# Optimization experiments

Measured on AMD Instinct MI355X. Metric: run time of the kernel, lower is better.

The kernel has to match this reference:

```python
import jax, jax.numpy as jnp
import numpy as np

B, C, H, W = 8, 256, 48, 48
EPS = 1e-5  # BatchNorm2d default eps


def setup_inputs() -> dict:
    key = jax.random.key(0)
    ks = jax.random.split(key, 8)
    return {
        "Q_feat_s": jax.random.normal(ks[0], (B, C, H, W), dtype=jnp.float32),
        "KV_feat_s": jax.random.normal(ks[1], (B, C, H, W), dtype=jnp.float32),
        "Wq": jax.random.normal(ks[2], (C, C), dtype=jnp.float32) * 0.02,
        "Wk": jax.random.normal(ks[3], (C, C), dtype=jnp.float32) * 0.02,
        "Wv": jax.random.normal(ks[4], (C, C), dtype=jnp.float32) * 0.02,
        "Wz": jax.random.normal(ks[5], (C, C), dtype=jnp.float32) * 0.02,
        "bn_gamma": jnp.ones((C,), dtype=jnp.float32),
        "bn_beta": jnp.zeros((C,), dtype=jnp.float32),
        "bn_mean": jax.random.normal(ks[6], (C,), dtype=jnp.float32) * 0.1,
        "bn_var": jax.random.uniform(ks[7], (C,), dtype=jnp.float32, minval=0.5, maxval=1.5),
    }


def reference(Q_feat_s, KV_feat_s, Wq, Wk, Wv, Wz, bn_gamma, bn_beta, bn_mean, bn_var):
    b, c, h, w = Q_feat_s.shape
    n = h * w
    # 1x1 convs == channel-mixing matmuls
    Q = jnp.einsum('oc,bchw->bohw', Wq, Q_feat_s).reshape(b, c, n)      # [B,C,N]
    K = jnp.einsum('oc,bchw->bohw', Wk, KV_feat_s).reshape(b, c, n)     # [B,C,N]
    V = jnp.einsum('oc,bchw->bohw', Wv, KV_feat_s).reshape(b, c, n)     # [B,C,N]
    # attn = (Q^T K)/N then @ V^T; linear (no softmax) so reassociate: Q^T (K V^T)/N
    KV = jnp.einsum('bcn,bdn->bcd', K, V) / n                           # [B,C,C]
    QKV = jnp.einsum('bcn,bcd->bdn', Q, KV)                             # [B,C,N]
    x = QKV.reshape(b, c, h, w)
    # W_z 1x1 conv + BatchNorm2d (inference / running stats)
    z = jnp.einsum('oc,bchw->bohw', Wz, x)
    inv = bn_gamma / jnp.sqrt(bn_var + EPS)
    z = z * inv[None, :, None, None] + (bn_beta - bn_mean * inv)[None, :, None, None]
    return z + Q_feat_s
```

## Files before the change

kernel.cpp:

```cpp
#include <hip/hip_runtime.h>

#define Bv 8
#define Cc 256
#define Nn 2304
#define EPS 1e-5f

typedef float f32x4 __attribute__((ext_vector_type(4)));
typedef __bf16 bf16x8 __attribute__((ext_vector_type(8)));

static __device__ __forceinline__ f32x4 mfma16(bf16x8 a, bf16x8 b, f32x4 c) {
    return __builtin_amdgcn_mfma_f32_16x16x32_bf16(a, b, c, 0, 0, 0);
}

static __device__ __forceinline__ bf16x8 cvt8(float4 a, float4 b) {
    bf16x8 r;
    r[0] = (__bf16)a.x; r[1] = (__bf16)a.y; r[2] = (__bf16)a.z; r[3] = (__bf16)a.w;
    r[4] = (__bf16)b.x; r[5] = (__bf16)b.y; r[6] = (__bf16)b.z; r[7] = (__bf16)b.w;
    return r;
}

static __device__ __forceinline__ bf16x8 load_cvt8(const float* __restrict__ p) {
    return cvt8(*(const float4*)p, *(const float4*)(p + 4));
}

static __device__ __forceinline__ bf16x8 load4_add_cvt8(
    const float* __restrict__ p0, const float* __restrict__ p1,
    const float* __restrict__ p2, const float* __restrict__ p3) {
    float4 x0 = *(const float4*)p0, x1 = *(const float4*)(p0 + 4);
    float4 y0 = *(const float4*)p1, y1 = *(const float4*)(p1 + 4);
    float4 z0 = *(const float4*)p2, z1 = *(const float4*)(p2 + 4);
    float4 w0 = *(const float4*)p3, w1 = *(const float4*)(p3 + 4);
    bf16x8 r;
    r[0] = (__bf16)(x0.x + y0.x + z0.x + w0.x);
    r[1] = (__bf16)(x0.y + y0.y + z0.y + w0.y);
    r[2] = (__bf16)(x0.z + y0.z + z0.z + w0.z);
    r[3] = (__bf16)(x0.w + y0.w + z0.w + w0.w);
    r[4] = (__bf16)(x1.x + y1.x + z1.x + w1.x);
    r[5] = (__bf16)(x1.y + y1.y + z1.y + w1.y);
    r[6] = (__bf16)(x1.z + y1.z + z1.z + w1.z);
    r[7] = (__bf16)(x1.w + y1.w + z1.w + w1.w);
    return r;
}

static __device__ __forceinline__ bf16x8 load_add_cvt8(const float* __restrict__ p0,
                                                       const float* __restrict__ p1) {
    float4 a0 = *(const float4*)p0;
    float4 a1 = *(const float4*)(p0 + 4);
    float4 b0 = *(const float4*)p1;
    float4 b1 = *(const float4*)(p1 + 4);
    bf16x8 r;
    r[0] = (__bf16)(a0.x + b0.x); r[1] = (__bf16)(a0.y + b0.y);
    r[2] = (__bf16)(a0.z + b0.z); r[3] = (__bf16)(a0.w + b0.w);
    r[4] = (__bf16)(a1.x + b1.x); r[5] = (__bf16)(a1.y + b1.y);
    r[6] = (__bf16)(a1.z + b1.z); r[7] = (__bf16)(a1.w + b1.w);
    return r;
}

__global__ __launch_bounds__(256) void k_front(
    const float* __restrict__ KVf,
    const float* __restrict__ Wq, const float* __restrict__ Wk,
    const float* __restrict__ Wv, const float* __restrict__ Wz,
    const float* __restrict__ gamma, const float* __restrict__ var_,
    unsigned short* __restrict__ Lb_us, unsigned short* __restrict__ Rtb_us,
    float* __restrict__ Spart) {
    __shared__ __align__(16) char smem[32768];
    int blk = blockIdx.x, tid = threadIdx.x;

    if (blk < 512) {
        __bf16 (*As)[72] = (__bf16 (*)[72])smem;
        __bf16 (*Bs)[72] = (__bf16 (*)[72])(smem + 9216);
        int b = blk & 7;
        int tt = (blk >> 3) & 15;
        int kc = blk >> 7;
        int tr = (tt >> 2) * 64, tc = (tt & 3) * 64;
        int k0 = kc * 576;
        int l = tid & 63, w = tid >> 6;
        int lr = l & 15, kofs = (l >> 4) * 8;
        int row = tid >> 2, c0 = (tid & 3) * 16;
        const float* Ap = KVf + ((size_t)b * Cc + tr + row) * Nn + k0 + c0;
        const float* Bp = KVf + ((size_t)b * Cc + tc + row) * Nn + k0 + c0;
        float4 fa0, fa1, fa2, fa3, fb0, fb1, fb2, fb3;
#define LD_TILE(ks) do { \
        const float* ap_ = Ap + (ks) * 64; \
        const float* bp_ = Bp + (ks) * 64; \
        fa0 = *(const float4*)ap_;         fa1 = *(const float4*)(ap_ + 4); \
        fa2 = *(const float4*)(ap_ + 8);   fa3 = *(const float4*)(ap_ + 12); \
        fb0 = *(const float4*)bp_;         fb1 = *(const float4*)(bp_ + 4); \
        fb2 = *(const float4*)(bp_ + 8);   fb3 = *(const float4*)(bp_ + 12); \
    } while (0)
        f32x4 zero = {0.f, 0.f, 0.f, 0.f};
        f32x4 acc[4] = {zero, zero, zero, zero};
        LD_TILE(0);
        for (int ks = 0; ks < 9; ++ks) {
            *(bf16x8*)&As[row][c0]     = cvt8(fa0, fa1);
            *(bf16x8*)&As[row][c0 + 8] = cvt8(fa2, fa3);
            *(bf16x8*)&Bs[row][c0]     = cvt8(fb0, fb1);
            *(bf16x8*)&Bs[row][c0 + 8] = cvt8(fb2, fb3);
            __syncthreads();
            if (ks < 8) LD_TILE(ks + 1);
#pragma unroll
            for (int kk = 0; kk < 64; kk += 32) {
                bf16x8 af = *(const bf16x8*)&As[w * 16 + lr][kk + kofs];
#pragma unroll
                for (int j = 0; j < 4; ++j) {
                    bf16x8 bb = *(const bf16x8*)&Bs[j * 16 + lr][kk + kofs];
                    acc[j] = mfma16(af, bb, acc[j]);
                }
            }
            __syncthreads();
        }
#undef LD_TILE
        float* Sp = Spart + ((size_t)kc * Bv + b) * 65536;
        int row0 = tr + w * 16 + ((l >> 4) << 2);
#pragma unroll
        for (int j = 0; j < 4; ++j) {
            int col = tc + j * 16 + lr;
#pragma unroll
            for (int r = 0; r < 4; ++r)
                Sp[(size_t)(row0 + r) * 256 + col] = acc[j][r];
        }
    } else {
        float* bufA = (float*)smem;
        float* bufB = bufA + 4096;
        __bf16* Lb  = (__bf16*)Lb_us;
        __bf16* Rtb = (__bf16*)Rtb_us;
        int wblk = blk - 512;
        bool isL = (wblk < 256);
        int t = isL ? wblk : wblk - 256;
        int tr = (t >> 4) * 16, tc = (t & 15) * 16;
        if (isL) {
            for (int idx = tid; idx < 4096; idx += 256) {
                int r = idx >> 8, m = idx & 255;
                bufA[idx] = Wz[(tr + r) * 256 + m];
            }
            for (int idx = tid; idx < 4096; idx += 256) {
                int m = idx >> 4, j = idx & 15;
                bufB[idx] = Wv[m * 256 + tc + j];
            }
        } else {
            for (int idx = tid; idx < 4096; idx += 256) {
                int o = idx >> 4, j = idx & 15;
                bufA[idx] = Wq[o * 256 + tr + j];
                bufB[idx] = Wk[o * 256 + tc + j];
            }
        }
        __syncthreads();
        int oo = tid >> 4, cc = tid & 15;
        float sum = 0.f;
        if (isL) {
#pragma unroll 8
            for (int m = 0; m < 256; ++m) sum += bufA[oo * 256 + m] * bufB[m * 16 + cc];
            int o = tr + oo;
            float inv = gamma[o] / sqrtf(var_[o] + EPS);
            Lb[o * 256 + tc + cc] = (__bf16)(inv * sum * (1.0f / (float)Nn));
        } else {
#pragma unroll 8
            for (int o = 0; o < 256; ++o) sum += bufA[o * 16 + oo] * bufB[o * 16 + cc];
            Rtb[(tr + oo) * 256 + tc + cc] = (__bf16)sum;
        }
    }
}

__global__ __launch_bounds__(256) void k_mid1(
    const unsigned short* __restrict__ Lb_us, const float* __restrict__ Spart,
    float* __restrict__ Tpart) {
    const __bf16* Lb = (const __bf16*)Lb_us;
    int blk = blockIdx.x;
    int b = blk & 7;
    int t = (blk >> 3) & 15;
    int kc = blk >> 7;
    int tr = (t >> 2) * 64, tc = (t & 3) * 64;
    int k0 = kc * 128;
    int tid = threadIdx.x, l = tid & 63, w = tid >> 6;
    int lr = l & 15, kofs = (l >> 4) * 8;
    const float* S0 = Spart + (size_t)(0 * Bv + b) * 65536;
    const float* S1 = Spart + (size_t)(1 * Bv + b) * 65536;
    const float* S2 = Spart + (size_t)(2 * Bv + b) * 65536;
    const float* S3 = Spart + (size_t)(3 * Bv + b) * 65536;
    f32x4 zero = {0.f, 0.f, 0.f, 0.f};
    f32x4 acc[4] = {zero, zero, zero, zero};
    int arow = tr + w * 16 + lr;
    for (int kk = 0; kk < 128; kk += 32) {
        bf16x8 af = *(const bf16x8*)&Lb[arow * 256 + k0 + kk + kofs];
#pragma unroll
        for (int j = 0; j < 4; ++j) {
            size_t boff = (size_t)(tc + j * 16 + lr) * 256 + k0 + kk + kofs;
            bf16x8 bb = load4_add_cvt8(S0 + boff, S1 + boff, S2 + boff, S3 + boff);
            acc[j] = mfma16(af, bb, acc[j]);
        }
    }
    float* Tp = Tpart + ((size_t)kc * Bv + b) * 65536;
    int row0 = tr + w * 16 + ((l >> 4) << 2);
#pragma unroll
    for (int j = 0; j < 4; ++j) {
        int col = tc + j * 16 + lr;
#pragma unroll
        for (int r = 0; r < 4; ++r)
            Tp[(size_t)(row0 + r) * 256 + col] = acc[j][r];
    }
}

__global__ __launch_bounds__(256) void k_mid2(
    const float* __restrict__ Tpart, const unsigned short* __restrict__ Rtb_us,
    unsigned short* __restrict__ Pb_us) {
    const __bf16* Rtb = (const __bf16*)Rtb_us;
    __bf16* Pb = (__bf16*)Pb_us;
    int blk = blockIdx.x;
    int b = blk & 7;
    int t = blk >> 3;
    int tr = (t >> 2) * 64, tc = (t & 3) * 64;
    int tid = threadIdx.x, l = tid & 63, w = tid >> 6;
    int lr = l & 15, kofs = (l >> 4) * 8;
    const float* T0 = Tpart + (size_t)b * 65536;
    const float* T1 = Tpart + (size_t)(Bv + b) * 65536;
    f32x4 zero = {0.f, 0.f, 0.f, 0.f};
    f32x4 acc[4] = {zero, zero, zero, zero};
    int arow = tr + w * 16 + lr;
    for (int kk = 0; kk < 256; kk += 32) {
        bf16x8 af = load_add_cvt8(&T0[(size_t)arow * 256 + kk + kofs],
                                  &T1[(size_t)arow * 256 + kk + kofs]);
#pragma unroll
        for (int j = 0; j < 4; ++j) {
            int brow = tc + j * 16 + lr;
            bf16x8 bb = *(const bf16x8*)&Rtb[brow * 256 + kk + kofs];
            acc[j] = mfma16(af, bb, acc[j]);
        }
    }
    __bf16* Pbb = Pb + ((size_t)b << 16);
    int row0 = tr + w * 16 + ((l >> 4) << 2);
#pragma unroll
    for (int j = 0; j < 4; ++j) {
        int col = tc + j * 16 + lr;
#pragma unroll
        for (int r = 0; r < 4; ++r)
            Pbb[(size_t)(row0 + r) * 256 + col] = (__bf16)acc[j][r];
    }
}

__global__ __launch_bounds__(512) void k_out(
    const unsigned short* __restrict__ Pb_us, const float* __restrict__ Qf,
    const float* __restrict__ gamma, const float* __restrict__ beta,
    const float* __restrict__ mean, const float* __restrict__ var_,
    float* __restrict__ out) {
    __shared__ __bf16 Qs[64][264];
    const __bf16* Pb = (const __bf16*)Pb_us;
    int bid = blockIdx.x;
    int b = bid & 7, nt = bid >> 3;
    int n0 = nt * 64;
    int tid = threadIdx.x, l = tid & 63, w = tid >> 6;
    int lr = l & 15, kofs = (l >> 4) * 8;

    const float* src = Qf + (size_t)b * Cc * Nn + n0;
    for (int idx = tid; idx < 4096; idx += 512) {
        int c = idx >> 4, ng = (idx & 15) << 2;
        float4 v = *(const float4*)(src + (size_t)c * Nn + ng);
        Qs[ng + 0][c] = (__bf16)v.x;
        Qs[ng + 1][c] = (__bf16)v.y;
        Qs[ng + 2][c] = (__bf16)v.z;
        Qs[ng + 3][c] = (__bf16)v.w;
    }
    __syncthreads();

    int obase = w * 32;
    const __bf16* A = Pb + ((size_t)b << 16);
    f32x4 zero = {0.f, 0.f, 0.f, 0.f};
    f32x4 acc[2][4];
#pragma unroll
    for (int i = 0; i < 2; ++i)
#pragma unroll
        for (int j = 0; j < 4; ++j) acc[i][j] = zero;

    for (int kk = 0; kk < 256; kk += 32) {
        bf16x8 af[2], bb[4];
#pragma unroll
        for (int i = 0; i < 2; ++i)
            af[i] = *(const bf16x8*)&A[(size_t)(obase + i * 16 + lr) * 256 + kk + kofs];
#pragma unroll
        for (int j = 0; j < 4; ++j)
            bb[j] = *(const bf16x8*)&Qs[j * 16 + lr][kk + kofs];
#pragma unroll
        for (int i = 0; i < 2; ++i)
#pragma unroll
            for (int j = 0; j < 4; ++j)
                acc[i][j] = mfma16(af[i], bb[j], acc[i][j]);
    }

    const float* Qfb = Qf + (size_t)b * Cc * Nn;
    float* outb = out + (size_t)b * Cc * Nn;
#pragma unroll
    for (int i = 0; i < 2; ++i) {
        int o0 = obase + i * 16 + ((l >> 4) << 2);
#pragma unroll
        for (int r = 0; r < 4; ++r) {
            int o = o0 + r;
            float inv = gamma[o] / sqrtf(var_[o] + EPS);
            float shift = beta[o] - mean[o] * inv;
#pragma unroll
            for (int j = 0; j < 4; ++j) {
                int n = n0 + j * 16 + lr;
                outb[(size_t)o * Nn + n] = acc[i][j][r] + shift + Qfb[(size_t)o * Nn + n];
            }
        }
    }
}

extern "C" void kernel_launch(void* const* d_in, const int* in_sizes, int n_in,
                              void* d_out, int out_size, void* d_ws, size_t ws_size,
                              hipStream_t stream) {
    (void)in_sizes; (void)n_in; (void)out_size; (void)ws_size;
    const float* Qf    = (const float*)d_in[0];
    const float* KVf   = (const float*)d_in[1];
    const float* Wq    = (const float*)d_in[2];
    const float* Wk    = (const float*)d_in[3];
    const float* Wv    = (const float*)d_in[4];
    const float* Wz    = (const float*)d_in[5];
    const float* gamma = (const float*)d_in[6];
    const float* beta  = (const float*)d_in[7];
    const float* mean  = (const float*)d_in[8];
    const float* var_  = (const float*)d_in[9];
    float* out = (float*)d_out;

    char* ws = (char*)d_ws;
    float* Spart        = (float*)ws;
    float* Tpart        = (float*)(ws + (8u << 20));
    unsigned short* Lb  = (unsigned short*)(ws + (12u << 20));
    unsigned short* Rtb = (unsigned short*)(ws + (12u << 20) + (128u << 10));
    unsigned short* Pb  = (unsigned short*)(ws + (12u << 20) + (256u << 10));

    k_front<<<1024, 256, 0, stream>>>(KVf, Wq, Wk, Wv, Wz, gamma, var_,
                                      Lb, Rtb, Spart);
    k_mid1<<<256, 256, 0, stream>>>(Lb, Spart, Tpart);
    k_mid2<<<128, 256, 0, stream>>>(Tpart, Rtb, Pb);
    k_out<<<288, 512, 0, stream>>>(Pb, Qf, gamma, beta, mean, var_, out);
}
```

Before: 156.5 us.

## Fuse two middle GEMM kernels via LDS row strips and halve k_out tile width

Merges k_mid1 and k_mid2 into one kernel. Each block computes a 16-row strip of the L·S product over the full K, stages it in shared memory as bf16, then multiplies by Rt to produce Pb. This removes the fp32 Tpart split-K partials round-trip through global memory and one launch, at the cost of fewer blocks (128) and each block re-reading the full S (summing four partials). The output kernel's N tile also shrinks from 64 to 32 columns, doubling its grid to 576 blocks for more parallelism while reloading Pb more often.

```diff
diff --git a/kernel.cpp b/kernel.cpp
--- a/kernel.cpp
+++ b/kernel.cpp
@@ -17,10 +17,6 @@
     r[0] = (__bf16)a.x; r[1] = (__bf16)a.y; r[2] = (__bf16)a.z; r[3] = (__bf16)a.w;
     r[4] = (__bf16)b.x; r[5] = (__bf16)b.y; r[6] = (__bf16)b.z; r[7] = (__bf16)b.w;
     return r;
-}
-
-static __device__ __forceinline__ bf16x8 load_cvt8(const float* __restrict__ p) {
-    return cvt8(*(const float4*)p, *(const float4*)(p + 4));
 }
 
 static __device__ __forceinline__ bf16x8 load4_add_cvt8(
@@ -39,20 +35,6 @@
     r[5] = (__bf16)(x1.y + y1.y + z1.y + w1.y);
     r[6] = (__bf16)(x1.z + y1.z + z1.z + w1.z);
     r[7] = (__bf16)(x1.w + y1.w + z1.w + w1.w);
-    return r;
-}
-
-static __device__ __forceinline__ bf16x8 load_add_cvt8(const float* __restrict__ p0,
-                                                       const float* __restrict__ p1) {
-    float4 a0 = *(const float4*)p0;
-    float4 a1 = *(const float4*)(p0 + 4);
-    float4 b0 = *(const float4*)p1;
-    float4 b1 = *(const float4*)(p1 + 4);
-    bf16x8 r;
-    r[0] = (__bf16)(a0.x + b0.x); r[1] = (__bf16)(a0.y + b0.y);
-    r[2] = (__bf16)(a0.z + b0.z); r[3] = (__bf16)(a0.w + b0.w);
-    r[4] = (__bf16)(a1.x + b1.x); r[5] = (__bf16)(a1.y + b1.y);
-    r[6] = (__bf16)(a1.z + b1.z); r[7] = (__bf16)(a1.w + b1.w);
     return r;
 }
 
@@ -161,16 +143,16 @@
     }
 }
 
-__global__ __launch_bounds__(256) void k_mid1(
+__global__ __launch_bounds__(256) void k_mid(
     const unsigned short* __restrict__ Lb_us, const float* __restrict__ Spart,
-    float* __restrict__ Tpart) {
+    const unsigned short* __restrict__ Rtb_us, unsigned short* __restrict__ Pb_us) {
+    __shared__ __bf16 Ts[16][264];
     const __bf16* Lb = (const __bf16*)Lb_us;
+    const __bf16* Rtb = (const __bf16*)Rtb_us;
+    __bf16* Pb = (__bf16*)Pb_us;
     int blk = blockIdx.x;
-    int b = blk & 7;
-    int t = (blk >> 3) & 15;
-    int kc = blk >> 7;
-    int tr = (t >> 2) * 64, tc = (t & 3) * 64;
-    int k0 = kc * 128;
+    int b = blk & 7, st = blk >> 3;
+    int r0 = st * 16;
     int tid = threadIdx.x, l = tid & 63, w = tid >> 6;
     int lr = l & 15, kofs = (l >> 4) * 8;
     const float* S0 = Spart + (size_t)(0 * Bv + b) * 65536;
@@ -178,62 +160,49 @@
     const float* S2 = Spart + (size_t)(2 * Bv + b) * 65536;
     const float* S3 = Spart + (size_t)(3 * Bv + b) * 65536;
     f32x4 zero = {0.f, 0.f, 0.f, 0.f};
-    f32x4 acc[4] = {zero, zero, zero, zero};
-    int arow = tr + w * 16 + lr;
-    for (int kk = 0; kk < 128; kk += 32) {
-        bf16x8 af = *(const bf16x8*)&Lb[arow * 256 + k0 + kk + kofs];
+
+    {
+        f32x4 acc[4] = {zero, zero, zero, zero};
+        for (int kk = 0; kk < 256; kk += 32) {
+            bf16x8 af = *(const bf16x8*)&Lb[(r0 + lr) * 256 + kk + kofs];
+#pragma unroll
+            for (int j = 0; j < 4; ++j) {
+                size_t boff = (size_t)(w * 64 + j * 16 + lr) * 256 + kk + kofs;
+                bf16x8 bb = load4_add_cvt8(S0 + boff, S1 + boff, S2 + boff, S3 + boff);
+                acc[j] = mfma16(af, bb, acc[j]);
+            }
+        }
+        int rloc = (l >> 4) << 2;
 #pragma unroll
         for (int j = 0; j < 4; ++j) {
-            size_t boff = (size_t)(tc + j * 16 + lr) * 256 + k0 + kk + kofs;
-            bf16x8 bb = load4_add_cvt8(S0 + boff, S1 + boff, S2 + boff, S3 + boff);
-            acc[j] = mfma16(af, bb, acc[j]);
-        }
-    }
-    float* Tp = Tpart + ((size_t)kc * Bv + b) * 65536;
-    int row0 = tr + w * 16 + ((l >> 4) << 2);
-#pragma unroll
-    for (int j = 0; j < 4; ++j) {
-        int col = tc + j * 16 + lr;
-#pragma unroll
-        for (int r = 0; r < 4; ++r)
-            Tp[(size_t)(row0 + r) * 256 + col] = acc[j][r];
-    }
-}
-
-__global__ __launch_bounds__(256) void k_mid2(
-    const float* __restrict__ Tpart, const unsigned short* __restrict__ Rtb_us,
-    unsigned short* __restrict__ Pb_us) {
-    const __bf16* Rtb = (const __bf16*)Rtb_us;
-    __bf16* Pb = (__bf16*)Pb_us;
-    int blk = blockIdx.x;
-    int b = blk & 7;
-    int t = blk >> 3;
-    int tr = (t >> 2) * 64, tc = (t & 3) * 64;
-    int tid = threadIdx.x, l = tid & 63, w = tid >> 6;
-    int lr = l & 15, kofs = (l >> 4) * 8;
-    const float* T0 = Tpart + (size_t)b * 65536;
-    const float* T1 = Tpart + (size_t)(Bv + b) * 65536;
-    f32x4 zero = {0.f, 0.f, 0.f, 0.f};
-    f32x4 acc[4] = {zero, zero, zero, zero};
-    int arow = tr + w * 16 + lr;
-    for (int kk = 0; kk < 256; kk += 32) {
-        bf16x8 af = load_add_cvt8(&T0[(size_t)arow * 256 + kk + kofs],
-                                  &T1[(size_t)arow * 256 + kk + kofs]);
+            int col = w * 64 + j * 16 + lr;
+#pragma unroll
+            for (int r = 0; r < 4; ++r)
+                Ts[rloc + r][col] = (__bf16)acc[j][r];
+        }
+    }
+    __syncthreads();
+
+    {
+        f32x4 acc[4] = {zero, zero, zero, zero};
+        for (int kk = 0; kk < 256; kk += 32) {
+            bf16x8 af = *(const bf16x8*)&Ts[lr][kk + kofs];
+#pragma unroll
+            for (int j = 0; j < 4; ++j) {
+                int brow = w * 64 + j * 16 + lr;
+                bf16x8 bb = *(const bf16x8*)&Rtb[brow * 256 + kk + kofs];
+                acc[j] = mfma16(af, bb, acc[j]);
+            }
+        }
+        __bf16* Pbb = Pb + ((size_t)b << 16);
+        int row0 = r0 + ((l >> 4) << 2);
 #pragma unroll
         for (int j = 0; j < 4; ++j) {
-            int brow = tc + j * 16 + lr;
-            bf16x8 bb = *(const bf16x8*)&Rtb[brow * 256 + kk + kofs];
-            acc[j] = mfma16(af, bb, acc[j]);
-        }
-    }
-    __bf16* Pbb = Pb + ((size_t)b << 16);
-    int row0 = tr + w * 16 + ((l >> 4) << 2);
-#pragma unroll
-    for (int j = 0; j < 4; ++j) {
-        int col = tc + j * 16 + lr;
-#pragma unroll
-        for (int r = 0; r < 4; ++r)
-            Pbb[(size_t)(row0 + r) * 256 + col] = (__bf16)acc[j][r];
+            int col = w * 64 + j * 16 + lr;
+#pragma unroll
+            for (int r = 0; r < 4; ++r)
+                Pbb[(size_t)(row0 + r) * 256 + col] = (__bf16)acc[j][r];
+        }
     }
 }
 
@@ -242,17 +211,17 @@
     const float* __restrict__ gamma, const float* __restrict__ beta,
     const float* __restrict__ mean, const float* __restrict__ var_,
     float* __restrict__ out) {
-    __shared__ __bf16 Qs[64][264];
+    __shared__ __bf16 Qs[32][264];
     const __bf16* Pb = (const __bf16*)Pb_us;
     int bid = blockIdx.x;
     int b = bid & 7, nt = bid >> 3;
-    int n0 = nt * 64;
+    int n0 = nt * 32;
     int tid = threadIdx.x, l = tid & 63, w = tid >> 6;
     int lr = l & 15, kofs = (l >> 4) * 8;
 
     const float* src = Qf + (size_t)b * Cc * Nn + n0;
-    for (int idx = tid; idx < 4096; idx += 512) {
-        int c = idx >> 4, ng = (idx & 15) << 2;
+    for (int idx = tid; idx < 2048; idx += 512) {
+        int c = idx >> 3, ng = (idx & 7) << 2;
         float4 v = *(const float4*)(src + (size_t)c * Nn + ng);
         Qs[ng + 0][c] = (__bf16)v.x;
         Qs[ng + 1][c] = (__bf16)v.y;
@@ -264,24 +233,25 @@
     int obase = w * 32;
     const __bf16* A = Pb + ((size_t)b << 16);
     f32x4 zero = {0.f, 0.f, 0.f, 0.f};
-    f32x4 acc[2][4];
+    f32x4 acc[2][2];
 #pragma unroll
     for (int i = 0; i < 2; ++i)
 #pragma unroll
-        for (int j = 0; j < 4; ++j) acc[i][j] = zero;
-
+        for (int j = 0; j < 2; ++j) acc[i][j] = zero;
+
+#pragma unroll 2
     for (int kk = 0; kk < 256; kk += 32) {
-        bf16x8 af[2], bb[4];
+        bf16x8 af[2], bb[2];
 #pragma unroll
         for (int i = 0; i < 2; ++i)
             af[i] = *(const bf16x8*)&A[(size_t)(obase + i * 16 + lr) * 256 + kk + kofs];
 #pragma unroll
-        for (int j = 0; j < 4; ++j)
+        for (int j = 0; j < 2; ++j)
             bb[j] = *(const bf16x8*)&Qs[j * 16 + lr][kk + kofs];
 #pragma unroll
         for (int i = 0; i < 2; ++i)
 #pragma unroll
-            for (int j = 0; j < 4; ++j)
+            for (int j = 0; j < 2; ++j)
                 acc[i][j] = mfma16(af[i], bb[j], acc[i][j]);
     }
 
@@ -296,7 +266,7 @@
             float inv = gamma[o] / sqrtf(var_[o] + EPS);
             float shift = beta[o] - mean[o] * inv;
 #pragma unroll
-            for (int j = 0; j < 4; ++j) {
+            for (int j = 0; j < 2; ++j) {
                 int n = n0 + j * 16 + lr;
                 outb[(size_t)o * Nn + n] = acc[i][j][r] + shift + Qfb[(size_t)o * Nn + n];
             }
@@ -322,14 +292,12 @@
 
     char* ws = (char*)d_ws;
     float* Spart        = (float*)ws;
-    float* Tpart        = (float*)(ws + (8u << 20));
-    unsigned short* Lb  = (unsigned short*)(ws + (12u << 20));
-    unsigned short* Rtb = (unsigned short*)(ws + (12u << 20) + (128u << 10));
-    unsigned short* Pb  = (unsigned short*)(ws + (12u << 20) + (256u << 10));
+    unsigned short* Lb  = (unsigned short*)(ws + (8u << 20));
+    unsigned short* Rtb = (unsigned short*)(ws + (8u << 20) + (128u << 10));
+    unsigned short* Pb  = (unsigned short*)(ws + (8u << 20) + (256u << 10));
 
     k_front<<<1024, 256, 0, stream>>>(KVf, Wq, Wk, Wv, Wz, gamma, var_,
                                       Lb, Rtb, Spart);
-    k_mid1<<<256, 256, 0, stream>>>(Lb, Spart, Tpart);
-    k_mid2<<<128, 256, 0, stream>>>(Tpart, Rtb, Pb);
-    k_out<<<288, 512, 0, stream>>>(Pb, Qf, gamma, beta, mean, var_, out);
-}
+    k_mid<<<128, 256, 0, stream>>>(Lb, Spart, Rtb, Pb);
+    k_out<<<576, 512, 0, stream>>>(Pb, Qf, gamma, beta, mean, var_, out);
+}
```

New measurement: 168.7 us. 1.08x slower.

## Split middle GEMMs over more blocks and take residual from shared-memory Q tile

Applied to the files above, without the earlier changes.

k_mid1 now splits the reduction dimension into four chunks instead of two, so it launches twice as many blocks. k_mid2 sums four fp32 partials and uses narrower 64x32 output tiles, which also doubles its grid; the workspace offsets are moved to make room for the larger partial buffer. In k_out the residual add reads Q from the bf16 shared-memory tile that was already staged, rather than re-reading fp32 Q_feat_s from global memory. This removes one full pass over the input but adds bf16 rounding error to the residual term, and the middle kernels write and read more partial data.

```diff
diff --git a/kernel.cpp b/kernel.cpp
--- a/kernel.cpp
+++ b/kernel.cpp
@@ -17,10 +17,6 @@
     r[0] = (__bf16)a.x; r[1] = (__bf16)a.y; r[2] = (__bf16)a.z; r[3] = (__bf16)a.w;
     r[4] = (__bf16)b.x; r[5] = (__bf16)b.y; r[6] = (__bf16)b.z; r[7] = (__bf16)b.w;
     return r;
-}
-
-static __device__ __forceinline__ bf16x8 load_cvt8(const float* __restrict__ p) {
-    return cvt8(*(const float4*)p, *(const float4*)(p + 4));
 }
 
 static __device__ __forceinline__ bf16x8 load4_add_cvt8(
@@ -39,20 +35,6 @@
     r[5] = (__bf16)(x1.y + y1.y + z1.y + w1.y);
     r[6] = (__bf16)(x1.z + y1.z + z1.z + w1.z);
     r[7] = (__bf16)(x1.w + y1.w + z1.w + w1.w);
-    return r;
-}
-
-static __device__ __forceinline__ bf16x8 load_add_cvt8(const float* __restrict__ p0,
-                                                       const float* __restrict__ p1) {
-    float4 a0 = *(const float4*)p0;
-    float4 a1 = *(const float4*)(p0 + 4);
-    float4 b0 = *(const float4*)p1;
-    float4 b1 = *(const float4*)(p1 + 4);
-    bf16x8 r;
-    r[0] = (__bf16)(a0.x + b0.x); r[1] = (__bf16)(a0.y + b0.y);
-    r[2] = (__bf16)(a0.z + b0.z); r[3] = (__bf16)(a0.w + b0.w);
-    r[4] = (__bf16)(a1.x + b1.x); r[5] = (__bf16)(a1.y + b1.y);
-    r[6] = (__bf16)(a1.z + b1.z); r[7] = (__bf16)(a1.w + b1.w);
     return r;
 }
 
@@ -170,7 +152,7 @@
     int t = (blk >> 3) & 15;
     int kc = blk >> 7;
     int tr = (t >> 2) * 64, tc = (t & 3) * 64;
-    int k0 = kc * 128;
+    int k0 = kc * 64;
     int tid = threadIdx.x, l = tid & 63, w = tid >> 6;
     int lr = l & 15, kofs = (l >> 4) * 8;
     const float* S0 = Spart + (size_t)(0 * Bv + b) * 65536;
@@ -180,7 +162,8 @@
     f32x4 zero = {0.f, 0.f, 0.f, 0.f};
     f32x4 acc[4] = {zero, zero, zero, zero};
     int arow = tr + w * 16 + lr;
-    for (int kk = 0; kk < 128; kk += 32) {
+#pragma unroll
+    for (int kk = 0; kk < 64; kk += 32) {
         bf16x8 af = *(const bf16x8*)&Lb[arow * 256 + k0 + kk + kofs];
 #pragma unroll
         for (int j = 0; j < 4; ++j) {
@@ -208,19 +191,21 @@
     int blk = blockIdx.x;
     int b = blk & 7;
     int t = blk >> 3;
-    int tr = (t >> 2) * 64, tc = (t & 3) * 64;
+    int tr = (t >> 3) * 64, tc = (t & 7) * 32;
     int tid = threadIdx.x, l = tid & 63, w = tid >> 6;
     int lr = l & 15, kofs = (l >> 4) * 8;
-    const float* T0 = Tpart + (size_t)b * 65536;
-    const float* T1 = Tpart + (size_t)(Bv + b) * 65536;
+    const float* T0 = Tpart + (size_t)(0 * Bv + b) * 65536;
+    const float* T1 = Tpart + (size_t)(1 * Bv + b) * 65536;
+    const float* T2 = Tpart + (size_t)(2 * Bv + b) * 65536;
+    const float* T3 = Tpart + (size_t)(3 * Bv + b) * 65536;
     f32x4 zero = {0.f, 0.f, 0.f, 0.f};
-    f32x4 acc[4] = {zero, zero, zero, zero};
+    f32x4 acc[2] = {zero, zero};
     int arow = tr + w * 16 + lr;
     for (int kk = 0; kk < 256; kk += 32) {
-        bf16x8 af = load_add_cvt8(&T0[(size_t)arow * 256 + kk + kofs],
-                                  &T1[(size_t)arow * 256 + kk + kofs]);
-#pragma unroll
-        for (int j = 0; j < 4; ++j) {
+        size_t aoff = (size_t)arow * 256 + kk + kofs;
+        bf16x8 af = load4_add_cvt8(T0 + aoff, T1 + aoff, T2 + aoff, T3 + aoff);
+#pragma unroll
+        for (int j = 0; j < 2; ++j) {
             int brow = tc + j * 16 + lr;
             bf16x8 bb = *(const bf16x8*)&Rtb[brow * 256 + kk + kofs];
             acc[j] = mfma16(af, bb, acc[j]);
@@ -229,7 +214,7 @@
     __bf16* Pbb = Pb + ((size_t)b << 16);
     int row0 = tr + w * 16 + ((l >> 4) << 2);
 #pragma unroll
-    for (int j = 0; j < 4; ++j) {
+    for (int j = 0; j < 2; ++j) {
         int col = tc + j * 16 + lr;
 #pragma unroll
         for (int r = 0; r < 4; ++r)
@@ -285,7 +270,6 @@
                 acc[i][j] = mfma16(af[i], bb[j], acc[i][j]);
     }
 
-    const float* Qfb = Qf + (size_t)b * Cc * Nn;
     float* outb = out + (size_t)b * Cc * Nn;
 #pragma unroll
     for (int i = 0; i < 2; ++i) {
@@ -297,8 +281,9 @@
             float shift = beta[o] - mean[o] * inv;
 #pragma unroll
             for (int j = 0; j < 4; ++j) {
-                int n = n0 + j * 16 + lr;
-                outb[(size_t)o * Nn + n] = acc[i][j][r] + shift + Qfb[(size_t)o * Nn + n];
+                int nl = j * 16 + lr;
+                float qres = (float)Qs[nl][o];
+                outb[(size_t)o * Nn + n0 + nl] = acc[i][j][r] + shift + qres;
             }
         }
     }
@@ -323,13 +308,13 @@
     char* ws = (char*)d_ws;
     float* Spart        = (float*)ws;
     float* Tpart        = (float*)(ws + (8u << 20));
-    unsigned short* Lb  = (unsigned short*)(ws + (12u << 20));
-    unsigned short* Rtb = (unsigned short*)(ws + (12u << 20) + (128u << 10));
-    unsigned short* Pb  = (unsigned short*)(ws + (12u << 20) + (256u << 10));
+    unsigned short* Lb  = (unsigned short*)(ws + (16u << 20));
+    unsigned short* Rtb = (unsigned short*)(ws + (16u << 20) + (128u << 10));
+    unsigned short* Pb  = (unsigned short*)(ws + (16u << 20) + (256u << 10));
 
     k_front<<<1024, 256, 0, stream>>>(KVf, Wq, Wk, Wv, Wz, gamma, var_,
                                       Lb, Rtb, Spart);
-    k_mid1<<<256, 256, 0, stream>>>(Lb, Spart, Tpart);
-    k_mid2<<<128, 256, 0, stream>>>(Tpart, Rtb, Pb);
+    k_mid1<<<512, 256, 0, stream>>>(Lb, Spart, Tpart);
+    k_mid2<<<256, 256, 0, stream>>>(Tpart, Rtb, Pb);
     k_out<<<288, 512, 0, stream>>>(Pb, Qf, gamma, beta, mean, var_, out);
 }
```

Result: no change. 155.5 us (-0.6%).
